# Performance work log

Hardware: AMD Instinct MI355X
Metric: run time of the kernel (lower is better)

## Reference

```python
import jax, jax.numpy as jnp
import numpy as np

V = 50257   # vocab_size
B = 32      # batch
T = 64      # blk_size (max seq len)
E = 256     # n_emb
H = 8       # n_heads
D = E // H  # head_size = 32
L = 8       # n_layers
F = 4 * E   # ffn hidden = 1024
EPS = 1e-5


def setup_inputs() -> dict:
    key = jax.random.key(0)
    ks = jax.random.split(key, 16)
    s = 0.02  # init std, matching _init_weights
    n = lambda k, shape: jax.random.normal(k, shape, dtype=jnp.float32) * s
    return {
        "ip": jax.random.randint(ks[0], (B, T), 0, V),
        "tok_emb": n(ks[1], (V, E)),
        "pos_emb": n(ks[2], (T, E)),
        # per-layer stacked params (leading axis = layer)
        "Wq": n(ks[3], (L, H, E, D)),
        "Wk": n(ks[4], (L, H, E, D)),
        "Wv": n(ks[5], (L, H, E, D)),
        "Wo": n(ks[6], (L, E, E)),
        "bo": jnp.zeros((L, E), jnp.float32),
        "ln1_g": jnp.ones((L, E), jnp.float32),
        "ln1_b": jnp.zeros((L, E), jnp.float32),
        "ln2_g": jnp.ones((L, E), jnp.float32),
        "ln2_b": jnp.zeros((L, E), jnp.float32),
        "W1": n(ks[7], (L, E, F)),
        "b1": jnp.zeros((L, F), jnp.float32),
        "W2": n(ks[8], (L, F, E)),
        "b2": jnp.zeros((L, E), jnp.float32),
        "lnf_g": jnp.ones((E,), jnp.float32),
        "lnf_b": jnp.zeros((E,), jnp.float32),
        "Wlm": n(ks[9], (E, V)),
        "blm": jnp.zeros((V,), jnp.float32),
    }


def _ln(x, g, b):
    m = jnp.mean(x, axis=-1, keepdims=True)
    v = jnp.var(x, axis=-1, keepdims=True)
    return (x - m) * jax.lax.rsqrt(v + EPS) * g + b


def _gpt(ip, tok_emb, pos_emb, Wq, Wk, Wv, Wo, bo, ln1_g, ln1_b, ln2_g, ln2_b,
         W1, b1, W2, b2, lnf_g, lnf_b, Wlm, blm):
    t = ip.shape[1]
    x = tok_emb[ip] + pos_emb[:t]                      # [B,T,E]
    mask = jnp.tril(jnp.ones((t, t), bool))            # causal
    scale = D ** -0.5

    def block(x, p):
        wq, wk, wv, wo, bo_, g1, b1_, g2, b2_, w1, bb1, w2, bb2 = p
        q = jnp.einsum('btc,hcd->bhtd', x, wq)
        k = jnp.einsum('btc,hcd->bhtd', x, wk)
        v = jnp.einsum('btc,hcd->bhtd', x, wv)
        scores = jnp.einsum('bhtd,bhsd->bhts', q, k) * scale
        scores = jnp.where(mask, scores, -jnp.inf)
        wei = jax.nn.softmax(scores, axis=-1)
        att = jnp.einsum('bhts,bhsd->bhtd', wei, v)
        att = att.transpose(0, 2, 1, 3).reshape(x.shape[0], t, E)  # concat heads
        x = _ln(x + (att @ wo + bo_), g1, b1_)          # post-norm residual
        y = jax.nn.relu(x @ w1 + bb1) @ w2 + bb2        # FFN
        x = _ln(x + y, g2, b2_)
        return x, None

    params = (Wq, Wk, Wv, Wo, bo, ln1_g, ln1_b, ln2_g, ln2_b, W1, b1, W2, b2)
    x, _ = jax.lax.scan(block, x, params)
    x = _ln(x, lnf_g, lnf_b)
    return x @ Wlm + blm                                # [B,T,V] logits


def reference(ip, tok_emb, pos_emb, Wq, Wk, Wv, Wo, bo, ln1_g, ln1_b, ln2_g,
              ln2_b, W1, b1, W2, b2, lnf_g, lnf_b, Wlm, blm):
    return _gpt(ip, tok_emb, pos_emb, Wq, Wk, Wv, Wo, bo, ln1_g, ln1_b,
                ln2_g, ln2_b, W1, b1, W2, b2, lnf_g, lnf_b, Wlm, blm)
```

## Files before the change

kernel.cpp:

```cpp
#include <hip/hip_runtime.h>

#define NB 32
#define NT 64
#define NE 256
#define NH 8
#define ND 32
#define NL 8
#define NF 1024
#define NV 50257
#define NVPAD 50304

typedef __bf16 bf16x8 __attribute__((ext_vector_type(8)));
typedef float f32x4 __attribute__((ext_vector_type(4)));

__device__ __forceinline__ float b2f(unsigned short h) {
  union { unsigned int u; float f; } c; c.u = ((unsigned int)h) << 16; return c.f;
}
__device__ __forceinline__ unsigned short f2b(float f) {
  union { float f; unsigned int u; } c; c.f = f;
  unsigned int u = c.u + 0x7FFFu + ((c.u >> 16) & 1u);
  return (unsigned short)(u >> 16);
}
__device__ __forceinline__ float ldf(const void* p, size_t i, int isbf) {
  return isbf ? b2f(((const unsigned short*)p)[i]) : ((const float*)p)[i];
}

__device__ __forceinline__ void gload16(const unsigned short* g, unsigned short* l) {
  __builtin_amdgcn_global_load_lds(
      (const __attribute__((address_space(1))) unsigned int*)g,
      (__attribute__((address_space(3))) unsigned int*)l, 16, 0, 0);
}

__global__ void detect_k(const unsigned int* __restrict__ probe, int* __restrict__ flag) {
  if (threadIdx.x == 0 && blockIdx.x == 0) {
    flag[0] = (probe[0] == 0x3F800000u) ? 0 : 1;
  }
}

__global__ __launch_bounds__(256)
void transpose_k(const void* __restrict__ srcv, unsigned short* __restrict__ dst,
                 const int* __restrict__ flag, int K, int N, int ZH,
                 long long src_ls, long long src_js, long long dst_ls, long long dst_js)
{
  __shared__ unsigned short tile[32][33];
  const int isbf = flag[0];
  const int z = blockIdx.z;
  const int l = z / ZH, j = z % ZH;
  const size_t sbase = (size_t)l * src_ls + (size_t)j * src_js;
  unsigned short* d = dst + (size_t)l * dst_ls + (size_t)j * dst_js;
  const int n0 = blockIdx.x * 32, k0 = blockIdx.y * 32;
  const int tx = threadIdx.x, ty = threadIdx.y;
#pragma unroll
  for (int i = 0; i < 4; ++i) {
    int k = k0 + ty + i * 8, n = n0 + tx;
    if (k < K && n < N) {
      size_t idx = sbase + (size_t)k * N + n;
      tile[ty + i * 8][tx] = isbf ? ((const unsigned short*)srcv)[idx]
                                  : f2b(((const float*)srcv)[idx]);
    }
  }
  __syncthreads();
#pragma unroll
  for (int i = 0; i < 4; ++i) {
    int n = n0 + ty + i * 8, k = k0 + tx;
    if (n < N && k < K) d[(size_t)n * K + k] = tile[tx][ty + i * 8];
  }
}

__global__ __launch_bounds__(256)
void embed_k(const int* __restrict__ ip, const void* __restrict__ te,
             const void* __restrict__ pe, const int* __restrict__ flag,
             float* __restrict__ x, unsigned short* __restrict__ xb)
{
  const int isbf = flag[0];
  const int i = blockIdx.x * 256 + threadIdx.x;
  const int tp = i >> 8, e = i & 255, t = tp & (NT - 1);
  const int id = ip[tp];
  float v = ldf(te, (size_t)id * NE + e, isbf) + ldf(pe, (size_t)t * NE + e, isbf);
  x[i] = v;
  xb[i] = f2b(v);
}

template<int BM, int BN, int BK, int WM, int WN, bool BIAS, bool RELU, int OUTMODE>
__global__ __launch_bounds__(256)
void gemm_bt(const unsigned short* __restrict__ A, const unsigned short* __restrict__ BT,
             const void* __restrict__ bias, int boff, const int* __restrict__ flag,
             void* __restrict__ Cv, int M, int N, int K, int ldc)
{
  static_assert((BM / WM) * (BN / WN) == 4, "4 waves");
  static_assert(BK == 64, "BK=64");
  __shared__ __align__(16) unsigned short As[BM * BK];
  __shared__ __align__(16) unsigned short Bs[BN * BK];
  const int tid = threadIdx.x;
  const int lane = tid & 63;
  const int wave = tid >> 6;
  const int m0 = blockIdx.y * BM;
  const int n0 = blockIdx.x * BN;
  constexpr int WAVES_N = BN / WN;
  const int wm = (wave / WAVES_N) * WM;
  const int wn = (wave % WAVES_N) * WN;
  constexpr int MT = WM / 16;
  constexpr int NTt = WN / 16;
  f32x4 acc[MT][NTt] = {};

  constexpr int AITERS = (BM * BK) / 2048;
  constexpr int BITERS = (BN * BK) / 2048;
  const int srow = tid >> 3;
  const int scol = (tid & 7) * 8;
  const int lc = lane & 15;
  const int lk = (lane >> 4) * 8;
  const int lr = (lane >> 4) * 4;

  for (int k0 = 0; k0 < K; k0 += BK) {
#pragma unroll
    for (int it = 0; it < AITERS; ++it)
      gload16(A + (size_t)(m0 + it * 32 + srow) * K + (k0 + scol), &As[it * 2048 + wave * 512]);
#pragma unroll
    for (int it = 0; it < BITERS; ++it)
      gload16(BT + (size_t)(n0 + it * 32 + srow) * K + (k0 + scol), &Bs[it * 2048 + wave * 512]);
    __syncthreads();
#pragma unroll
    for (int ks = 0; ks < BK; ks += 32) {
      bf16x8 afr[MT], bfr[NTt];
#pragma unroll
      for (int i = 0; i < MT; ++i)
        afr[i] = *(const bf16x8*)&As[(wm + i * 16 + lc) * BK + ks + lk];
#pragma unroll
      for (int j = 0; j < NTt; ++j)
        bfr[j] = *(const bf16x8*)&Bs[(wn + j * 16 + lc) * BK + ks + lk];
#pragma unroll
      for (int i = 0; i < MT; ++i)
#pragma unroll
        for (int j = 0; j < NTt; ++j)
          acc[i][j] = __builtin_amdgcn_mfma_f32_16x16x32_bf16(afr[i], bfr[j], acc[i][j], 0, 0, 0);
    }
    __syncthreads();
  }

  const int isbf = (BIAS || OUTMODE == 2) ? flag[0] : 1;
#pragma unroll
  for (int i = 0; i < MT; ++i) {
#pragma unroll
    for (int j = 0; j < NTt; ++j) {
      const int col = n0 + wn + j * 16 + lc;
      if (col < N) {
        float bv = BIAS ? ldf(bias, (size_t)(boff + col), isbf) : 0.0f;
#pragma unroll
        for (int q = 0; q < 4; ++q) {
          const int row = m0 + wm + i * 16 + lr + q;
          float v = acc[i][j][q] + bv;
          if (RELU) v = fmaxf(v, 0.0f);
          const size_t idx = (size_t)row * ldc + col;
          if (OUTMODE == 1) ((float*)Cv)[idx] = v;
          else if (OUTMODE == 0) ((unsigned short*)Cv)[idx] = f2b(v);
          else { if (isbf) ((unsigned short*)Cv)[idx] = f2b(v); else ((float*)Cv)[idx] = v; }
        }
      }
    }
  }
}

__global__ __launch_bounds__(64)
void attn_k(const unsigned short* __restrict__ qkv, unsigned short* __restrict__ att)
{
  const int bh = blockIdx.x, b = bh >> 3, h = bh & 7;
  __shared__ float Q[NT][ND], Kc[NT][ND], Vc[NT][ND];
  const int tid = threadIdx.x;
  const unsigned short* base = qkv + (size_t)(b * NT) * (3 * NE) + h * ND;
  for (int i = tid; i < NT * ND; i += 64) {
    const int s = i >> 5, d = i & 31;
    const unsigned short* row = base + s * (3 * NE) + d;
    Q[s][d]  = b2f(row[0]);
    Kc[s][d] = b2f(row[NE]);
    Vc[s][d] = b2f(row[2 * NE]);
  }
  __syncthreads();
  const int t = tid;
  float q[ND];
#pragma unroll
  for (int d = 0; d < ND; ++d) q[d] = Q[t][d] * 0.17677669529663689f;
  float mx = -1e30f;
  for (int s = 0; s <= t; ++s) {
    const float4* kp = (const float4*)&Kc[s][0];
    float dot = 0.0f;
#pragma unroll
    for (int c = 0; c < 8; ++c) {
      float4 kv = kp[c];
      dot += q[c*4+0]*kv.x + q[c*4+1]*kv.y + q[c*4+2]*kv.z + q[c*4+3]*kv.w;
    }
    mx = fmaxf(mx, dot);
  }
  float sum = 0.0f;
  float acc[ND] = {};
  for (int s = 0; s <= t; ++s) {
    const float4* kp = (const float4*)&Kc[s][0];
    float dot = 0.0f;
#pragma unroll
    for (int c = 0; c < 8; ++c) {
      float4 kv = kp[c];
      dot += q[c*4+0]*kv.x + q[c*4+1]*kv.y + q[c*4+2]*kv.z + q[c*4+3]*kv.w;
    }
    const float e = __expf(dot - mx);
    sum += e;
    const float4* vp = (const float4*)&Vc[s][0];
#pragma unroll
    for (int c = 0; c < 8; ++c) {
      float4 vv = vp[c];
      acc[c*4+0] += e*vv.x; acc[c*4+1] += e*vv.y; acc[c*4+2] += e*vv.z; acc[c*4+3] += e*vv.w;
    }
  }
  const float inv = 1.0f / sum;
  unsigned short* op = att + (size_t)(b * NT + t) * NE + h * ND;
#pragma unroll
  for (int d = 0; d < ND; ++d) op[d] = f2b(acc[d] * inv);
}

template<bool RES>
__global__ __launch_bounds__(256)
void ln_k(const float* __restrict__ xin, const float* __restrict__ yin,
          const void* __restrict__ gv, const void* __restrict__ bv, int goff,
          const int* __restrict__ flag,
          float* __restrict__ xout_f, unsigned short* __restrict__ xout_b)
{
  const int isbf = flag[0];
  const int tok = blockIdx.x, e = threadIdx.x;
  float v = xin[tok * NE + e];
  if (RES) v += yin[tok * NE + e];
  float s = v, s2 = v * v;
#pragma unroll
  for (int off = 32; off > 0; off >>= 1) {
    s  += __shfl_down(s, off);
    s2 += __shfl_down(s2, off);
  }
  __shared__ float red[10];
  const int wv = e >> 6, ln = e & 63;
  if (ln == 0) { red[wv] = s; red[4 + wv] = s2; }
  __syncthreads();
  if (e == 0) {
    const float ts = red[0] + red[1] + red[2] + red[3];
    const float t2 = red[4] + red[5] + red[6] + red[7];
    const float m = ts * (1.0f / NE);
    const float var = t2 * (1.0f / NE) - m * m;
    red[8] = m; red[9] = rsqrtf(var + 1e-5f);
  }
  __syncthreads();
  const float m = red[8], r = red[9];
  const float o = (v - m) * r * ldf(gv, (size_t)(goff + e), isbf) + ldf(bv, (size_t)(goff + e), isbf);
  if (xout_f) xout_f[tok * NE + e] = o;
  xout_b[tok * NE + e] = f2b(o);
}

extern "C" void kernel_launch(void* const* d_in, const int* in_sizes, int n_in,
                              void* d_out, int out_size, void* d_ws, size_t ws_size,
                              hipStream_t stream) {
  const int* ip      = (const int*)d_in[0];
  const void* tok_emb = d_in[1];
  const void* pos_emb = d_in[2];
  const void* Wq = d_in[3];
  const void* Wk = d_in[4];
  const void* Wv = d_in[5];
  const void* Wo = d_in[6];
  const void* bo = d_in[7];
  const void* ln1_g = d_in[8];
  const void* ln1_b = d_in[9];
  const void* ln2_g = d_in[10];
  const void* ln2_b = d_in[11];
  const void* W1 = d_in[12];
  const void* b1 = d_in[13];
  const void* W2 = d_in[14];
  const void* b2 = d_in[15];
  const void* lnf_g = d_in[16];
  const void* lnf_b = d_in[17];
  const void* Wlm = d_in[18];
  const void* blm = d_in[19];

  const int M = NB * NT;

  int* flag = (int*)d_ws;
  unsigned short* base = (unsigned short*)d_ws + 32;
  unsigned short* xb   = base;
  unsigned short* xf   = xb   + (size_t)M * NE;
  unsigned short* qkv  = xf   + (size_t)M * NE;
  unsigned short* att  = qkv  + (size_t)M * 3 * NE;
  unsigned short* hbuf = att  + (size_t)M * NE;
  float*          x    = (float*)(hbuf + (size_t)M * NF);
  float*          y    = x + (size_t)M * NE;
  unsigned short* WqkvT = (unsigned short*)(y + (size_t)M * NE);
  unsigned short* WoT  = WqkvT + (size_t)NL * 768 * NE;
  unsigned short* W1T  = WoT   + (size_t)NL * NE * NE;
  unsigned short* W2T  = W1T   + (size_t)NL * NF * NE;
  unsigned short* WlmT = W2T   + (size_t)NL * NE * NF;

  detect_k<<<dim3(1), dim3(64), 0, stream>>>((const unsigned int*)ln1_g, flag);

  dim3 tb(32, 8, 1);
  transpose_k<<<dim3(1, 8, NL * NH), tb, 0, stream>>>(Wq, WqkvT,             flag, NE, ND, NH, 65536LL, 8192LL, 196608LL, 8192LL);
  transpose_k<<<dim3(1, 8, NL * NH), tb, 0, stream>>>(Wk, WqkvT + NE * NE,   flag, NE, ND, NH, 65536LL, 8192LL, 196608LL, 8192LL);
  transpose_k<<<dim3(1, 8, NL * NH), tb, 0, stream>>>(Wv, WqkvT + 2*NE*NE,   flag, NE, ND, NH, 65536LL, 8192LL, 196608LL, 8192LL);
  transpose_k<<<dim3(8, 8, NL),  tb, 0, stream>>>(Wo, WoT,  flag, NE, NE, 1, 65536LL, 0LL, 65536LL, 0LL);
  transpose_k<<<dim3(32, 8, NL), tb, 0, stream>>>(W1, W1T,  flag, NE, NF, 1, 262144LL, 0LL, 262144LL, 0LL);
  transpose_k<<<dim3(8, 32, NL), tb, 0, stream>>>(W2, W2T,  flag, NF, NE, 1, 262144LL, 0LL, 262144LL, 0LL);
  transpose_k<<<dim3((NV + 31) / 32, 8, 1), tb, 0, stream>>>(Wlm, WlmT, flag, NE, NV, 1, 0LL, 0LL, 0LL, 0LL);

  embed_k<<<dim3(M), dim3(256), 0, stream>>>(ip, tok_emb, pos_emb, flag, x, xb);

  for (int l = 0; l < NL; ++l) {
    gemm_bt<64, 64, 64, 32, 32, false, false, 0><<<dim3(768 / 64, M / 64), dim3(256), 0, stream>>>(
        xb, WqkvT + (size_t)l * 768 * NE, nullptr, 0, flag, qkv, M, 768, NE, 768);
    attn_k<<<dim3(NB * NH), dim3(64), 0, stream>>>(qkv, att);
    gemm_bt<64, 64, 64, 32, 32, true, false, 1><<<dim3(NE / 64, M / 64), dim3(256), 0, stream>>>(
        att, WoT + (size_t)l * NE * NE, bo, l * NE, flag, y, M, NE, NE, NE);
    ln_k<true><<<dim3(M), dim3(256), 0, stream>>>(x, y, ln1_g, ln1_b, l * NE, flag, x, xb);
    gemm_bt<64, 64, 64, 32, 32, true, true, 0><<<dim3(NF / 64, M / 64), dim3(256), 0, stream>>>(
        xb, W1T + (size_t)l * NF * NE, b1, l * NF, flag, hbuf, M, NF, NE, NF);
    gemm_bt<64, 64, 64, 32, 32, true, false, 1><<<dim3(NE / 64, M / 64), dim3(256), 0, stream>>>(
        hbuf, W2T + (size_t)l * NE * NF, b2, l * NE, flag, y, M, NE, NF, NE);
    ln_k<true><<<dim3(M), dim3(256), 0, stream>>>(x, y, ln2_g, ln2_b, l * NE, flag, x, xb);
  }

  ln_k<false><<<dim3(M), dim3(256), 0, stream>>>(x, nullptr, lnf_g, lnf_b, 0, flag, nullptr, xf);

  gemm_bt<128, 128, 64, 64, 64, true, false, 2><<<dim3(NVPAD / 128, M / 128), dim3(256), 0, stream>>>(
      xf, WlmT, blm, 0, flag, d_out, M, NV, NE, NV);
}
```

Baseline: 1.292 ms.

## Fuse residual LayerNorm into projection GEMMs and split attention across waves

Folds the residual add and LayerNorm into the output-projection and FFN-down GEMM kernels with a full-row tile, removing separate LN launches and the fp32 intermediate buffer. Attention now uses four waves that each handle a key slice and then merge partial softmax statistics. The weight transposes are merged into one launch and the flag-detection kernel is replaced by an inline probe read. The fused GEMM launches fewer blocks and uses more shared memory, which lowers parallelism.

```diff
diff --git a/kernel.cpp b/kernel.cpp
--- a/kernel.cpp
+++ b/kernel.cpp
@@ -24,6 +24,9 @@
 __device__ __forceinline__ float ldf(const void* p, size_t i, int isbf) {
   return isbf ? b2f(((const unsigned short*)p)[i]) : ((const float*)p)[i];
 }
+__device__ __forceinline__ int get_isbf(const unsigned int* probe) {
+  return (probe[0] == 0x3F800000u) ? 0 : 1;
+}
 
 __device__ __forceinline__ void gload16(const unsigned short* g, unsigned short* l) {
   __builtin_amdgcn_global_load_lds(
@@ -31,48 +34,79 @@
       (__attribute__((address_space(3))) unsigned int*)l, 16, 0, 0);
 }
 
-__global__ void detect_k(const unsigned int* __restrict__ probe, int* __restrict__ flag) {
-  if (threadIdx.x == 0 && blockIdx.x == 0) {
-    flag[0] = (probe[0] == 0x3F800000u) ? 0 : 1;
+__global__ __launch_bounds__(256)
+void transpose_weights_k(const void* __restrict__ Wq, const void* __restrict__ Wk,
+                         const void* __restrict__ Wv, const void* __restrict__ Wo,
+                         const void* __restrict__ W1, const void* __restrict__ W2,
+                         const unsigned int* __restrict__ probe,
+                         unsigned short* __restrict__ WqkvT, unsigned short* __restrict__ WoT,
+                         unsigned short* __restrict__ W1T, unsigned short* __restrict__ W2T)
+{
+  __shared__ unsigned short tile[32][33];
+  const int isbf = get_isbf(probe);
+  const int z = blockIdx.z, x = blockIdx.x;
+  const void* src; unsigned short* dst; int K, N, k0, n0;
+  size_t soff, doff;
+  if (x < 192) {
+    const int t = x >> 6, r = x & 63, h = r >> 3, ky = r & 7;
+    src = (t == 0) ? Wq : ((t == 1) ? Wk : Wv);
+    soff = (size_t)z * 65536 + (size_t)h * 8192; K = 256; N = 32; k0 = ky * 32; n0 = 0;
+    dst = WqkvT; doff = (size_t)z * 196608 + (size_t)(t * 256 + h * 32) * 256;
+  } else if (x < 256) {
+    const int r = x - 192, ny = r >> 3, ky = r & 7;
+    src = Wo; soff = (size_t)z * 65536; K = 256; N = 256; k0 = ky * 32; n0 = ny * 32;
+    dst = WoT; doff = (size_t)z * 65536;
+  } else if (x < 512) {
+    const int r = x - 256, ny = r >> 3, ky = r & 7;
+    src = W1; soff = (size_t)z * 262144; K = 256; N = 1024; k0 = ky * 32; n0 = ny * 32;
+    dst = W1T; doff = (size_t)z * 262144;
+  } else {
+    const int r = x - 512, ky = r >> 3, ny = r & 7;
+    src = W2; soff = (size_t)z * 262144; K = 1024; N = 256; k0 = ky * 32; n0 = ny * 32;
+    dst = W2T; doff = (size_t)z * 262144;
+  }
+  const int tx = threadIdx.x, ty = threadIdx.y;
+#pragma unroll
+  for (int i = 0; i < 4; ++i) {
+    const int k = k0 + ty + i * 8, n = n0 + tx;
+    tile[ty + i * 8][tx] = f2b(ldf(src, soff + (size_t)k * N + n, isbf));
+  }
+  __syncthreads();
+#pragma unroll
+  for (int i = 0; i < 4; ++i) {
+    const int n = n0 + ty + i * 8, k = k0 + tx;
+    dst[doff + (size_t)n * K + k] = tile[tx][ty + i * 8];
   }
 }
 
 __global__ __launch_bounds__(256)
 void transpose_k(const void* __restrict__ srcv, unsigned short* __restrict__ dst,
-                 const int* __restrict__ flag, int K, int N, int ZH,
-                 long long src_ls, long long src_js, long long dst_ls, long long dst_js)
+                 const unsigned int* __restrict__ probe, int K, int N)
 {
   __shared__ unsigned short tile[32][33];
-  const int isbf = flag[0];
-  const int z = blockIdx.z;
-  const int l = z / ZH, j = z % ZH;
-  const size_t sbase = (size_t)l * src_ls + (size_t)j * src_js;
-  unsigned short* d = dst + (size_t)l * dst_ls + (size_t)j * dst_js;
+  const int isbf = get_isbf(probe);
   const int n0 = blockIdx.x * 32, k0 = blockIdx.y * 32;
   const int tx = threadIdx.x, ty = threadIdx.y;
 #pragma unroll
   for (int i = 0; i < 4; ++i) {
-    int k = k0 + ty + i * 8, n = n0 + tx;
-    if (k < K && n < N) {
-      size_t idx = sbase + (size_t)k * N + n;
-      tile[ty + i * 8][tx] = isbf ? ((const unsigned short*)srcv)[idx]
-                                  : f2b(((const float*)srcv)[idx]);
-    }
+    const int k = k0 + ty + i * 8, n = n0 + tx;
+    if (k < K && n < N)
+      tile[ty + i * 8][tx] = f2b(ldf(srcv, (size_t)k * N + n, isbf));
   }
   __syncthreads();
 #pragma unroll
   for (int i = 0; i < 4; ++i) {
-    int n = n0 + ty + i * 8, k = k0 + tx;
-    if (n < N && k < K) d[(size_t)n * K + k] = tile[tx][ty + i * 8];
+    const int n = n0 + ty + i * 8, k = k0 + tx;
+    if (n < N && k < K) dst[(size_t)n * K + k] = tile[tx][ty + i * 8];
   }
 }
 
 __global__ __launch_bounds__(256)
 void embed_k(const int* __restrict__ ip, const void* __restrict__ te,
-             const void* __restrict__ pe, const int* __restrict__ flag,
+             const void* __restrict__ pe, const unsigned int* __restrict__ probe,
              float* __restrict__ x, unsigned short* __restrict__ xb)
 {
-  const int isbf = flag[0];
+  const int isbf = get_isbf(probe);
   const int i = blockIdx.x * 256 + threadIdx.x;
   const int tp = i >> 8, e = i & 255, t = tp & (NT - 1);
   const int id = ip[tp];
@@ -84,7 +118,7 @@
 template<int BM, int BN, int BK, int WM, int WN, bool BIAS, bool RELU, int OUTMODE>
 __global__ __launch_bounds__(256)
 void gemm_bt(const unsigned short* __restrict__ A, const unsigned short* __restrict__ BT,
-             const void* __restrict__ bias, int boff, const int* __restrict__ flag,
+             const void* __restrict__ bias, int boff, const unsigned int* __restrict__ probe,
              void* __restrict__ Cv, int M, int N, int K, int ldc)
 {
   static_assert((BM / WM) * (BN / WN) == 4, "4 waves");
@@ -137,7 +171,8 @@
     __syncthreads();
   }
 
-  const int isbf = (BIAS || OUTMODE == 2) ? flag[0] : 1;
+  int isbf = 1;
+  if constexpr (BIAS || OUTMODE == 2) isbf = get_isbf(probe);
 #pragma unroll
   for (int i = 0; i < MT; ++i) {
 #pragma unroll
@@ -160,14 +195,90 @@
   }
 }
 
-__global__ __launch_bounds__(64)
+__global__ __launch_bounds__(256)
+void gemm_ln_k(const unsigned short* __restrict__ A, const unsigned short* __restrict__ BT,
+               const void* __restrict__ bias, int boff,
+               const void* __restrict__ g, const void* __restrict__ b, int goff,
+               const unsigned int* __restrict__ probe, const float* __restrict__ xres,
+               float* __restrict__ xout, unsigned short* __restrict__ xbout, int K)
+{
+  __shared__ __align__(16) unsigned short As[32 * 64];
+  __shared__ __align__(16) unsigned short Bs[256 * 64];
+  __shared__ float vbuf[32][257];
+  const int isbf = get_isbf(probe);
+  const int tid = threadIdx.x, lane = tid & 63, wave = tid >> 6;
+  const int m0 = blockIdx.x * 32;
+  const int wn = wave * 64;
+  const int srow = tid >> 3, scol = (tid & 7) * 8;
+  const int lc = lane & 15, lk = (lane >> 4) * 8, lr = (lane >> 4) * 4;
+  f32x4 acc[2][4] = {};
+
+  for (int k0 = 0; k0 < K; k0 += 64) {
+    gload16(A + (size_t)(m0 + srow) * K + (k0 + scol), &As[wave * 512]);
+#pragma unroll
+    for (int it = 0; it < 8; ++it)
+      gload16(BT + (size_t)(it * 32 + srow) * K + (k0 + scol), &Bs[it * 2048 + wave * 512]);
+    __syncthreads();
+#pragma unroll
+    for (int ks = 0; ks < 64; ks += 32) {
+      bf16x8 afr[2], bfr[4];
+#pragma unroll
+      for (int i = 0; i < 2; ++i)
+        afr[i] = *(const bf16x8*)&As[(i * 16 + lc) * 64 + ks + lk];
+#pragma unroll
+      for (int j = 0; j < 4; ++j)
+        bfr[j] = *(const bf16x8*)&Bs[(wn + j * 16 + lc) * 64 + ks + lk];
+#pragma unroll
+      for (int i = 0; i < 2; ++i)
+#pragma unroll
+        for (int j = 0; j < 4; ++j)
+          acc[i][j] = __builtin_amdgcn_mfma_f32_16x16x32_bf16(afr[i], bfr[j], acc[i][j], 0, 0, 0);
+    }
+    __syncthreads();
+  }
+
+#pragma unroll
+  for (int i = 0; i < 2; ++i) {
+#pragma unroll
+    for (int j = 0; j < 4; ++j) {
+      const int col = wn + j * 16 + lc;
+      const float bv = ldf(bias, (size_t)(boff + col), isbf);
+#pragma unroll
+      for (int q = 0; q < 4; ++q) {
+        const int row = i * 16 + lr + q;
+        vbuf[row][col] = acc[i][j][q] + bv + xres[(size_t)(m0 + row) * NE + col];
+      }
+    }
+  }
+  __syncthreads();
+
+  const int row = tid >> 3, lo = tid & 7;
+  float s = 0.0f, s2 = 0.0f;
+  for (int c = lo; c < 256; c += 8) { const float v = vbuf[row][c]; s += v; s2 += v * v; }
+#pragma unroll
+  for (int off = 4; off > 0; off >>= 1) { s += __shfl_xor(s, off); s2 += __shfl_xor(s2, off); }
+  const float m = s * (1.0f / NE);
+  const float var = s2 * (1.0f / NE) - m * m;
+  const float r = rsqrtf(var + 1e-5f);
+  for (int c = lo; c < 256; c += 8) {
+    const float o = (vbuf[row][c] - m) * r * ldf(g, (size_t)(goff + c), isbf)
+                    + ldf(b, (size_t)(goff + c), isbf);
+    const size_t idx = (size_t)(m0 + row) * NE + c;
+    xout[idx] = o;
+    xbout[idx] = f2b(o);
+  }
+}
+
+__global__ __launch_bounds__(256)
 void attn_k(const unsigned short* __restrict__ qkv, unsigned short* __restrict__ att)
 {
   const int bh = blockIdx.x, b = bh >> 3, h = bh & 7;
   __shared__ float Q[NT][ND], Kc[NT][ND], Vc[NT][ND];
-  const int tid = threadIdx.x;
+  __shared__ float pm[4][NT], pl[4][NT];
+  __shared__ float pacc[4][NT][ND + 1];
+  const int tid = threadIdx.x, wv = tid >> 6, l = tid & 63;
   const unsigned short* base = qkv + (size_t)(b * NT) * (3 * NE) + h * ND;
-  for (int i = tid; i < NT * ND; i += 64) {
+  for (int i = tid; i < NT * ND; i += 256) {
     const int s = i >> 5, d = i & 31;
     const unsigned short* row = base + s * (3 * NE) + d;
     Q[s][d]  = b2f(row[0]);
@@ -175,29 +286,31 @@
     Vc[s][d] = b2f(row[2 * NE]);
   }
   __syncthreads();
-  const int t = tid;
+  const int t = l;
   float q[ND];
 #pragma unroll
   for (int d = 0; d < ND; ++d) q[d] = Q[t][d] * 0.17677669529663689f;
+  const int s0 = wv * 16;
+  const int s1 = min(s0 + 16, t + 1);
   float mx = -1e30f;
-  for (int s = 0; s <= t; ++s) {
+  for (int s = s0; s < s1; ++s) {
     const float4* kp = (const float4*)&Kc[s][0];
     float dot = 0.0f;
 #pragma unroll
     for (int c = 0; c < 8; ++c) {
-      float4 kv = kp[c];
+      const float4 kv = kp[c];
       dot += q[c*4+0]*kv.x + q[c*4+1]*kv.y + q[c*4+2]*kv.z + q[c*4+3]*kv.w;
     }
     mx = fmaxf(mx, dot);
   }
   float sum = 0.0f;
   float acc[ND] = {};
-  for (int s = 0; s <= t; ++s) {
+  for (int s = s0; s < s1; ++s) {
     const float4* kp = (const float4*)&Kc[s][0];
     float dot = 0.0f;
 #pragma unroll
     for (int c = 0; c < 8; ++c) {
-      float4 kv = kp[c];
+      const float4 kv = kp[c];
       dot += q[c*4+0]*kv.x + q[c*4+1]*kv.y + q[c*4+2]*kv.z + q[c*4+3]*kv.w;
     }
     const float e = __expf(dot - mx);
@@ -205,27 +318,41 @@
     const float4* vp = (const float4*)&Vc[s][0];
 #pragma unroll
     for (int c = 0; c < 8; ++c) {
-      float4 vv = vp[c];
+      const float4 vv = vp[c];
       acc[c*4+0] += e*vv.x; acc[c*4+1] += e*vv.y; acc[c*4+2] += e*vv.z; acc[c*4+3] += e*vv.w;
     }
   }
-  const float inv = 1.0f / sum;
-  unsigned short* op = att + (size_t)(b * NT + t) * NE + h * ND;
-#pragma unroll
-  for (int d = 0; d < ND; ++d) op[d] = f2b(acc[d] * inv);
-}
-
-template<bool RES>
-__global__ __launch_bounds__(256)
-void ln_k(const float* __restrict__ xin, const float* __restrict__ yin,
-          const void* __restrict__ gv, const void* __restrict__ bv, int goff,
-          const int* __restrict__ flag,
-          float* __restrict__ xout_f, unsigned short* __restrict__ xout_b)
-{
-  const int isbf = flag[0];
+  pm[wv][t] = mx; pl[wv][t] = sum;
+#pragma unroll
+  for (int d = 0; d < ND; ++d) pacc[wv][t][d] = acc[d];
+  __syncthreads();
+
+  const int mt = tid >> 2, jj = tid & 3;
+  float M = -1e30f;
+#pragma unroll
+  for (int w = 0; w < 4; ++w) M = fmaxf(M, pm[w][mt]);
+  float ew[4], L = 0.0f;
+#pragma unroll
+  for (int w = 0; w < 4; ++w) { ew[w] = __expf(pm[w][mt] - M); L += pl[w][mt] * ew[w]; }
+  const float inv = 1.0f / L;
+  unsigned short* op = att + (size_t)(b * NT + mt) * NE + h * ND + jj * 8;
+#pragma unroll
+  for (int dd = 0; dd < 8; ++dd) {
+    float o = 0.0f;
+#pragma unroll
+    for (int w = 0; w < 4; ++w) o += pacc[w][mt][jj * 8 + dd] * ew[w];
+    op[dd] = f2b(o * inv);
+  }
+}
+
+__global__ __launch_bounds__(256)
+void lnf_k(const float* __restrict__ xin, const void* __restrict__ gv,
+           const void* __restrict__ bv, const unsigned int* __restrict__ probe,
+           unsigned short* __restrict__ xout_b)
+{
+  const int isbf = get_isbf(probe);
   const int tok = blockIdx.x, e = threadIdx.x;
-  float v = xin[tok * NE + e];
-  if (RES) v += yin[tok * NE + e];
+  const float v = xin[tok * NE + e];
   float s = v, s2 = v * v;
 #pragma unroll
   for (int off = 32; off > 0; off >>= 1) {
@@ -245,15 +372,14 @@
   }
   __syncthreads();
   const float m = red[8], r = red[9];
-  const float o = (v - m) * r * ldf(gv, (size_t)(goff + e), isbf) + ldf(bv, (size_t)(goff + e), isbf);
-  if (xout_f) xout_f[tok * NE + e] = o;
+  const float o = (v - m) * r * ldf(gv, (size_t)e, isbf) + ldf(bv, (size_t)e, isbf);
   xout_b[tok * NE + e] = f2b(o);
 }
 
 extern "C" void kernel_launch(void* const* d_in, const int* in_sizes, int n_in,
                               void* d_out, int out_size, void* d_ws, size_t ws_size,
                               hipStream_t stream) {
-  const int* ip      = (const int*)d_in[0];
+  const int* ip = (const int*)d_in[0];
   const void* tok_emb = d_in[1];
   const void* pos_emb = d_in[2];
   const void* Wq = d_in[3];
@@ -273,53 +399,45 @@
   const void* lnf_b = d_in[17];
   const void* Wlm = d_in[18];
   const void* blm = d_in[19];
+  const unsigned int* probe = (const unsigned int*)ln1_g;
 
   const int M = NB * NT;
 
-  int* flag = (int*)d_ws;
-  unsigned short* base = (unsigned short*)d_ws + 32;
-  unsigned short* xb   = base;
+  unsigned short* xb   = (unsigned short*)d_ws;
   unsigned short* xf   = xb   + (size_t)M * NE;
   unsigned short* qkv  = xf   + (size_t)M * NE;
   unsigned short* att  = qkv  + (size_t)M * 3 * NE;
   unsigned short* hbuf = att  + (size_t)M * NE;
   float*          x    = (float*)(hbuf + (size_t)M * NF);
-  float*          y    = x + (size_t)M * NE;
-  unsigned short* WqkvT = (unsigned short*)(y + (size_t)M * NE);
+  unsigned short* WqkvT = (unsigned short*)(x + (size_t)M * NE);
   unsigned short* WoT  = WqkvT + (size_t)NL * 768 * NE;
   unsigned short* W1T  = WoT   + (size_t)NL * NE * NE;
   unsigned short* W2T  = W1T   + (size_t)NL * NF * NE;
   unsigned short* WlmT = W2T   + (size_t)NL * NE * NF;
 
-  detect_k<<<dim3(1), dim3(64), 0, stream>>>((const unsigned int*)ln1_g, flag);
-
   dim3 tb(32, 8, 1);
-  transpose_k<<<dim3(1, 8, NL * NH), tb, 0, stream>>>(Wq, WqkvT,             flag, NE, ND, NH, 65536LL, 8192LL, 196608LL, 8192LL);
-  transpose_k<<<dim3(1, 8, NL * NH), tb, 0, stream>>>(Wk, WqkvT + NE * NE,   flag, NE, ND, NH, 65536LL, 8192LL, 196608LL, 8192LL);
-  transpose_k<<<dim3(1, 8, NL * NH), tb, 0, stream>>>(Wv, WqkvT + 2*NE*NE,   flag, NE, ND, NH, 65536LL, 8192LL, 196608LL, 8192LL);
-  transpose_k<<<dim3(8, 8, NL),  tb, 0, stream>>>(Wo, WoT,  flag, NE, NE, 1, 65536LL, 0LL, 65536LL, 0LL);
-  transpose_k<<<dim3(32, 8, NL), tb, 0, stream>>>(W1, W1T,  flag, NE, NF, 1, 262144LL, 0LL, 262144LL, 0LL);
-  transpose_k<<<dim3(8, 32, NL), tb, 0, stream>>>(W2, W2T,  flag, NF, NE, 1, 262144LL, 0LL, 262144LL, 0LL);
-  transpose_k<<<dim3((NV + 31) / 32, 8, 1), tb, 0, stream>>>(Wlm, WlmT, flag, NE, NV, 1, 0LL, 0LL, 0LL, 0LL);
-
-  embed_k<<<dim3(M), dim3(256), 0, stream>>>(ip, tok_emb, pos_emb, flag, x, xb);
+  transpose_weights_k<<<dim3(768, 1, NL), tb, 0, stream>>>(
+      Wq, Wk, Wv, Wo, W1, W2, probe, WqkvT, WoT, W1T, W2T);
+  transpose_k<<<dim3((NV + 31) / 32, NE / 32, 1), tb, 0, stream>>>(Wlm, WlmT, probe, NE, NV);
+
+  embed_k<<<dim3(M), dim3(256), 0, stream>>>(ip, tok_emb, pos_emb, probe, x, xb);
 
   for (int l = 0; l < NL; ++l) {
     gemm_bt<64, 64, 64, 32, 32, false, false, 0><<<dim3(768 / 64, M / 64), dim3(256), 0, stream>>>(
-        xb, WqkvT + (size_t)l * 768 * NE, nullptr, 0, flag, qkv, M, 768, NE, 768);
-    attn_k<<<dim3(NB * NH), dim3(64), 0, stream>>>(qkv, att);
-    gemm_bt<64, 64, 64, 32, 32, true, false, 1><<<dim3(NE / 64, M / 64), dim3(256), 0, stream>>>(
-        att, WoT + (size_t)l * NE * NE, bo, l * NE, flag, y, M, NE, NE, NE);
-    ln_k<true><<<dim3(M), dim3(256), 0, stream>>>(x, y, ln1_g, ln1_b, l * NE, flag, x, xb);
+        xb, WqkvT + (size_t)l * 768 * NE, nullptr, 0, probe, qkv, M, 768, NE, 768);
+    attn_k<<<dim3(NB * NH), dim3(256), 0, stream>>>(qkv, att);
+    gemm_ln_k<<<dim3(M / 32), dim3(256), 0, stream>>>(
+        att, WoT + (size_t)l * NE * NE, bo, l * NE, ln1_g, ln1_b, l * NE,
+        probe, x, x, xb, NE);
     gemm_bt<64, 64, 64, 32, 32, true, true, 0><<<dim3(NF / 64, M / 64), dim3(256), 0, stream>>>(
-        xb, W1T + (size_t)l * NF * NE, b1, l * NF, flag, hbuf, M, NF, NE, NF);
-    gemm_bt<64, 64, 64, 32, 32, true, false, 1><<<dim3(NE / 64, M / 64), dim3(256), 0, stream>>>(
-        hbuf, W2T + (size_t)l * NE * NF, b2, l * NE, flag, y, M, NE, NF, NE);
-    ln_k<true><<<dim3(M), dim3(256), 0, stream>>>(x, y, ln2_g, ln2_b, l * NE, flag, x, xb);
-  }
-
-  ln_k<false><<<dim3(M), dim3(256), 0, stream>>>(x, nullptr, lnf_g, lnf_b, 0, flag, nullptr, xf);
+        xb, W1T + (size_t)l * NF * NE, b1, l * NF, probe, hbuf, M, NF, NE, NF);
+    gemm_ln_k<<<dim3(M / 32), dim3(256), 0, stream>>>(
+        hbuf, W2T + (size_t)l * NE * NF, b2, l * NE, ln2_g, ln2_b, l * NE,
+        probe, x, x, xb, NF);
+  }
+
+  lnf_k<<<dim3(M), dim3(256), 0, stream>>>(x, lnf_g, lnf_b, probe, xf);
 
   gemm_bt<128, 128, 64, 64, 64, true, false, 2><<<dim3(NVPAD / 128, M / 128), dim3(256), 0, stream>>>(
-      xf, WlmT, blm, 0, flag, d_out, M, NV, NE, NV);
-}
+      xf, WlmT, blm, 0, probe, d_out, M, NV, NE, NV);
+}
```

Result: faster. 1.238 ms (-4.2%).
